# Kernel optimization log

Hardware: AMD Instinct MI355X
Metric: run time of the kernel (lower is better)

The kernel has to match this reference:

```python
import jax, jax.numpy as jnp
import numpy as np

DT = 10.0          # ms per step
T_STEPS = 120      # rollout length
THRESHOLD = 0.5
MIX = 0.0          # competition_mix (buffer, default 0.0)
EPS_TOTAL = 1e-6
EPS_SLOPE = 1e-3
NOISE_SEED = 42


def setup_inputs() -> dict:
    key = jax.random.key(0)
    B, C = 65536, 4
    logits = jax.random.normal(key, (B, C), dtype=jnp.float32)
    return {
        "logits": logits,
        "input_scale": jnp.float32(0.25),
        "leak": jnp.full((C,), 0.08, dtype=jnp.float32),
        "self_excitation": jnp.full((C,), 0.12, dtype=jnp.float32),
        "inhibition": jnp.float32(0.08),
        "competition_gain": jnp.float32(1.0),
        "noise_std": jnp.float32(0.02),
        "evidence_w": jnp.float32(1.0),   # evidence_proj: Linear(1,1) weight
        "evidence_b": jnp.float32(0.0),   # evidence_proj bias
    }


def _forward(logits, input_scale, leak, self_excitation, inhibition,
             competition_gain, noise_std, evidence_w, evidence_b):
    B, C = logits.shape
    # momentary evidence: scale, center, softplus, 1x1 linear
    centered = logits * input_scale
    centered = centered - jnp.mean(centered, axis=1, keepdims=True)
    evidence = jax.nn.softplus(centered) * evidence_w + evidence_b  # (B, C)

    lk = jax.nn.softplus(leak)                # (C,)
    se = jax.nn.softplus(self_excitation)     # (C,)
    inhib = jax.nn.softplus(inhibition)       # ()
    cgain = jax.nn.softplus(competition_gain) # ()
    nstd = jax.nn.softplus(noise_std)         # ()

    keys = jax.random.split(jax.random.key(NOISE_SEED), T_STEPS)

    def step(acc, k):
        total = jnp.sum(acc, axis=1, keepdims=True)      # (B, 1)
        total_other = total - acc                        # (B, C)
        normalized_other = total_other / (total + EPS_TOTAL)
        competition = (1.0 - MIX) * total_other + MIX * cgain * normalized_other
        drive = evidence + se * acc - inhib * competition - lk * acc
        noise = jax.random.normal(k, (B, C), dtype=jnp.float32) * nstd
        dsdt = jax.nn.softplus(drive + noise) - acc
        acc_new = jnp.maximum(acc + 0.2 * dsdt, 0.0)     # clamp(min=0)
        return acc_new, (acc_new, dsdt)

    acc0 = jnp.zeros((B, C), dtype=jnp.float32)
    _, (traj, dsdt_traj) = jax.lax.scan(step, acc0, keys)
    traj = jnp.transpose(traj, (1, 0, 2))           # (B, T, C)
    dsdt_traj = jnp.transpose(dsdt_traj, (1, 0, 2)) # (B, T, C)

    # DiffDecisionMultiClass: first threshold crossing per class, with
    # linear interpolation using dsdt (slope = 0.2*dsdt per step) so the
    # decision time is differentiable via the implicit-function gradient.
    diff = traj - THRESHOLD                          # (B, T, C)
    crossed = diff > 0.0
    any_c = jnp.any(crossed, axis=1)                 # (B, C)
    idx = jnp.argmax(crossed, axis=1)                # (B, C) first crossing step
    idx = jnp.where(any_c, idx, T_STEPS - 1)

    diff_c = jnp.take_along_axis(diff, idx[:, None, :], axis=1)[:, 0, :]       # (B, C)
    slope = 0.2 * jnp.take_along_axis(dsdt_traj, idx[:, None, :], axis=1)[:, 0, :]
    slope_safe = jnp.where(slope >= 0.0,
                           jnp.maximum(slope, EPS_SLOPE),
                           jnp.minimum(slope, -EPS_SLOPE))
    # continuous crossing time in steps (gradient flows through diff_c only)
    t_cont = idx.astype(jnp.float32) - diff_c / jax.lax.stop_gradient(slope_safe)
    times_ms = jnp.where(any_c, t_cont * DT, jnp.float32(T_STEPS * DT))
    return times_ms / 1000.0  # seconds, (B, C)


def reference(logits, input_scale, leak, self_excitation, inhibition,
              competition_gain, noise_std, evidence_w, evidence_b):
    return _forward(logits, input_scale, leak, self_excitation, inhibition,
                    competition_gain, noise_std, evidence_w, evidence_b)
```

## Files before the change

### kernel.cpp

```cpp
#include <hip/hip_runtime.h>
#include <cstdint>

#define TSTEPS 120
#define KPAD   (TSTEPS + 4)

typedef unsigned int u32;

constexpr u32 rotl_c(u32 x, u32 r) { return (x << r) | (x >> (32u - r)); }

struct KeyTab { u32 w[KPAD][2]; };

constexpr KeyTab make_tab() {
    KeyTab kt{};
    for (int t = 0; t < KPAD; ++t) {
        const u32 k0 = 0u, k1 = 42u, ks2 = k0 ^ k1 ^ 0x1BD11BDAu;
        u32 x0 = k0, x1 = (u32)t + k1;
        const u32 rA[4] = {13u, 15u, 26u, 6u};
        const u32 rB[4] = {17u, 29u, 16u, 24u};
        for (int g = 0; g < 5; ++g) {
            const u32* rr = (g % 2 == 0) ? rA : rB;
            for (int i = 0; i < 4; ++i) { x0 += x1; x1 = rotl_c(x1, rr[i]); x1 ^= x0; }
            switch (g) {
                case 0: x0 += k1;  x1 += ks2 + 1u; break;
                case 1: x0 += ks2; x1 += k0 + 2u;  break;
                case 2: x0 += k0;  x1 += k1 + 3u;  break;
                case 3: x0 += k1;  x1 += ks2 + 4u; break;
                case 4: x0 += ks2; x1 += k0 + 5u;  break;
            }
        }
        kt.w[t][0] = x0; kt.w[t][1] = x1;
    }
    return kt;
}

__constant__ KeyTab KT = make_tab();

__device__ __forceinline__ u32 rotl32(u32 x, u32 r) { return (x << r) | (x >> (32u - r)); }

__device__ __forceinline__ float qxor1(float x) {
    return __int_as_float(__builtin_amdgcn_update_dpp(0, __float_as_int(x), 0xB1, 0xF, 0xF, true));
}
__device__ __forceinline__ float qxor2(float x) {
    return __int_as_float(__builtin_amdgcn_update_dpp(0, __float_as_int(x), 0x4E, 0xF, 0xF, true));
}

__device__ __forceinline__ float softplus_s(float x) {
    const float LOG2E = 1.4426950408889634f, LN2 = 0.6931471805599453f;
    float e = __builtin_amdgcn_exp2f(-fabsf(x) * LOG2E);
    return fmaxf(x, 0.0f) + __builtin_amdgcn_logf(1.0f + e) * LN2;
}

__device__ __forceinline__ float erfinv_fast(float x) {
    const float LN2 = 0.6931471805599453f;
    float t = __builtin_fmaf(-x, x, 1.0f);
    float w = __builtin_amdgcn_logf(t) * (-LN2);
    float wa = w - 2.5f;
    float p = 2.81022636e-08f;
    p = fmaf(p, wa, 3.43273939e-07f);
    p = fmaf(p, wa, -3.5233877e-06f);
    p = fmaf(p, wa, -4.39150654e-06f);
    p = fmaf(p, wa, 0.00021858087f);
    p = fmaf(p, wa, -0.00125372503f);
    p = fmaf(p, wa, -0.00417768164f);
    p = fmaf(p, wa, 0.246640727f);
    p = fmaf(p, wa, 1.50140941f);
    if (__any(w >= 5.0f)) {
        float wb = __builtin_amdgcn_sqrtf(w) - 3.0f;
        float q = -0.000200214257f;
        q = fmaf(q, wb, 0.000100950558f);
        q = fmaf(q, wb, 0.00134934322f);
        q = fmaf(q, wb, -0.00367342844f);
        q = fmaf(q, wb, 0.00573950773f);
        q = fmaf(q, wb, -0.0076224613f);
        q = fmaf(q, wb, 0.00943887047f);
        q = fmaf(q, wb, 1.00167406f);
        q = fmaf(q, wb, 2.83297682f);
        p = (w < 5.0f) ? p : q;
    }
    return p * x;
}

__device__ __forceinline__ u32 tf_bits(int t, u32 c) {
    const u32 k0 = KT.w[t][0], k1 = KT.w[t][1];
    const u32 ks2 = k0 ^ k1 ^ 0x1BD11BDAu;
    const u32 i1 = ks2 + 1u, i2 = k0 + 2u, i3 = k1 + 3u, i4 = ks2 + 4u, i5 = k0 + 5u;
    u32 x0 = k0, x1 = c + k1;
#define TF_R(r) { x0 += x1; x1 = rotl32(x1, (r)); x1 ^= x0; }
    TF_R(13u) TF_R(15u) TF_R(26u) TF_R(6u)
    x0 += k1;  x1 += i1;
    TF_R(17u) TF_R(29u) TF_R(16u) TF_R(24u)
    x0 += ks2; x1 += i2;
    TF_R(13u) TF_R(15u) TF_R(26u) TF_R(6u)
    x0 += k0;  x1 += i3;
    TF_R(17u) TF_R(29u) TF_R(16u) TF_R(24u)
    x0 += k1;  x1 += i4;
    TF_R(13u) TF_R(15u) TF_R(26u) TF_R(6u)
    x0 += ks2; x1 += i5;
#undef TF_R
    return x0 ^ x1;
}

__global__ __launch_bounds__(256, 4) void accrace_kernel(
    const float* __restrict__ logits,
    const float* __restrict__ g_input_scale,
    const float* __restrict__ g_leak,
    const float* __restrict__ g_se,
    const float* __restrict__ g_inhib,
    const float* __restrict__ g_nstd,
    const float* __restrict__ g_ew,
    const float* __restrict__ g_eb,
    float* __restrict__ out, int n)
{
    const int tid = threadIdx.x;
    const int j = blockIdx.x * 256 + tid;
    if (j >= n) return;
    const int c = tid & 3;

    const float input_scale = g_input_scale[0];
    const float lkc   = softplus_s(g_leak[c]);
    const float sec   = softplus_s(g_se[c]);
    const float inhib = softplus_s(g_inhib[0]);
    const float nstd  = softplus_s(g_nstd[0]);
    const float ew = g_ew[0], eb = g_eb[0];

    const float gain   = sec + inhib - lkc;
    const float minhib = -inhib;
    const float SQ2N   = 1.41421356237309515f * nstd;
    const float LO     = -0.99999994f;

    const float xs = logits[j] * input_scale;
    float m = xs + qxor1(xs); m = (m + qxor2(m)) * 0.25f;
    const float evd = softplus_s(xs - m) * ew + eb;

    const u32 ctr = (u32)j;

    float nz;
    u32 bitsa;
    {
        const u32 b0 = tf_bits(0, ctr);
        const float F0 = __uint_as_float((b0 >> 9) | 0x3F800000u);
        const float u0 = fmaxf(fmaf(F0, 2.0f, -3.0f), LO);
        nz = erfinv_fast(u0) * SQ2N;
        bitsa = tf_bits(1, ctr);
    }

    float acc = 0.0f, dfx = 0.0f, slx = 0.0f;
    int idxv = -1;

#pragma unroll 4
    for (int t = 0; t < TSTEPS; ++t) {
        float s1  = acc + qxor1(acc);
        float tot = s1 + qxor2(s1);
        const float dr = fmaf(acc, gain, fmaf(tot, minhib, evd));
        const float sp = softplus_s(dr + nz);
        const float ds = sp - acc;
        const float an = fmaxf(fmaf(ds, 0.2f, acc), 0.0f);

        const bool cr = (idxv < 0) & (an > 0.5f);
        idxv = cr ? t : idxv;
        dfx  = cr ? an : dfx;
        slx  = cr ? ds : slx;
        acc = an;

        const float F = __uint_as_float((bitsa >> 9) | 0x3F800000u);
        const float u = fmaxf(fmaf(F, 2.0f, -3.0f), LO);
        nz = erfinv_fast(u) * SQ2N;
        bitsa = tf_bits(t + 2, ctr);
    }

    float o = 1.2f;
    if (idxv >= 0) {
        const float sl = 0.2f * slx;
        const float ss = (sl >= 0.0f) ? fmaxf(sl, 1e-3f) : fminf(sl, -1e-3f);
        o = (((float)idxv - (dfx - 0.5f) / ss) * 10.0f) / 1000.0f;
    }
    out[j] = o;
}

extern "C" void kernel_launch(void* const* d_in, const int* in_sizes, int n_in,
                              void* d_out, int out_size, void* d_ws, size_t ws_size,
                              hipStream_t stream) {
    const float* logits       = (const float*)d_in[0];
    const float* input_scale  = (const float*)d_in[1];
    const float* leak         = (const float*)d_in[2];
    const float* self_excit   = (const float*)d_in[3];
    const float* inhibition   = (const float*)d_in[4];
    const float* noise_std    = (const float*)d_in[6];
    const float* evidence_w   = (const float*)d_in[7];
    const float* evidence_b   = (const float*)d_in[8];

    const int n = in_sizes[0];
    const int threads = 256;
    const int blocks = (n + threads - 1) / threads;
    accrace_kernel<<<blocks, threads, 0, stream>>>(
        logits, input_scale, leak, self_excit, inhibition,
        noise_std, evidence_w, evidence_b, (float*)d_out, n);
}
```

Measured before the change: 88.73 us.

## Batch noise generation per 15-step tile and make erfinv branchless

```diff
diff --git a/kernel.cpp b/kernel.cpp
--- a/kernel.cpp
+++ b/kernel.cpp
@@ -2,17 +2,18 @@
 #include <cstdint>
 
 #define TSTEPS 120
-#define KPAD   (TSTEPS + 4)
+#define TTILE  15
+#define NTILES (TSTEPS / TTILE)
 
 typedef unsigned int u32;
 
 constexpr u32 rotl_c(u32 x, u32 r) { return (x << r) | (x >> (32u - r)); }
 
-struct KeyTab { u32 w[KPAD][2]; };
+struct KeyTab { u32 w[TSTEPS][2]; };
 
 constexpr KeyTab make_tab() {
     KeyTab kt{};
-    for (int t = 0; t < KPAD; ++t) {
+    for (int t = 0; t < TSTEPS; ++t) {
         const u32 k0 = 0u, k1 = 42u, ks2 = k0 ^ k1 ^ 0x1BD11BDAu;
         u32 x0 = k0, x1 = (u32)t + k1;
         const u32 rA[4] = {13u, 15u, 26u, 6u};
@@ -37,6 +38,10 @@
 
 __device__ __forceinline__ u32 rotl32(u32 x, u32 r) { return (x << r) | (x >> (32u - r)); }
 
+__device__ __forceinline__ float rfl(float x) {
+    return __int_as_float(__builtin_amdgcn_readfirstlane(__float_as_int(x)));
+}
+
 __device__ __forceinline__ float qxor1(float x) {
     return __int_as_float(__builtin_amdgcn_update_dpp(0, __float_as_int(x), 0xB1, 0xF, 0xF, true));
 }
@@ -50,33 +55,22 @@
     return fmaxf(x, 0.0f) + __builtin_amdgcn_logf(1.0f + e) * LN2;
 }
 
-__device__ __forceinline__ float erfinv_fast(float x) {
+__device__ __forceinline__ float erfinv_bl(float x) {
     const float LN2 = 0.6931471805599453f;
     float t = __builtin_fmaf(-x, x, 1.0f);
     float w = __builtin_amdgcn_logf(t) * (-LN2);
     float wa = w - 2.5f;
-    float p = 2.81022636e-08f;
-    p = fmaf(p, wa, 3.43273939e-07f);
-    p = fmaf(p, wa, -3.5233877e-06f);
-    p = fmaf(p, wa, -4.39150654e-06f);
-    p = fmaf(p, wa, 0.00021858087f);
-    p = fmaf(p, wa, -0.00125372503f);
-    p = fmaf(p, wa, -0.00417768164f);
-    p = fmaf(p, wa, 0.246640727f);
-    p = fmaf(p, wa, 1.50140941f);
-    if (__any(w >= 5.0f)) {
-        float wb = __builtin_amdgcn_sqrtf(w) - 3.0f;
-        float q = -0.000200214257f;
-        q = fmaf(q, wb, 0.000100950558f);
-        q = fmaf(q, wb, 0.00134934322f);
-        q = fmaf(q, wb, -0.00367342844f);
-        q = fmaf(q, wb, 0.00573950773f);
-        q = fmaf(q, wb, -0.0076224613f);
-        q = fmaf(q, wb, 0.00943887047f);
-        q = fmaf(q, wb, 1.00167406f);
-        q = fmaf(q, wb, 2.83297682f);
-        p = (w < 5.0f) ? p : q;
-    }
+    float wb = __builtin_amdgcn_sqrtf(w) - 3.0f;
+    float p = 2.81022636e-08f;           float q = -0.000200214257f;
+    p = fmaf(p, wa, 3.43273939e-07f);    q = fmaf(q, wb, 0.000100950558f);
+    p = fmaf(p, wa, -3.5233877e-06f);    q = fmaf(q, wb, 0.00134934322f);
+    p = fmaf(p, wa, -4.39150654e-06f);   q = fmaf(q, wb, -0.00367342844f);
+    p = fmaf(p, wa, 0.00021858087f);     q = fmaf(q, wb, 0.00573950773f);
+    p = fmaf(p, wa, -0.00125372503f);    q = fmaf(q, wb, -0.0076224613f);
+    p = fmaf(p, wa, -0.00417768164f);    q = fmaf(q, wb, 0.00943887047f);
+    p = fmaf(p, wa, 0.246640727f);       q = fmaf(q, wb, 1.00167406f);
+    p = fmaf(p, wa, 1.50140941f);        q = fmaf(q, wb, 2.83297682f);
+    p = (w < 5.0f) ? p : q;
     return p * x;
 }
 
@@ -119,13 +113,13 @@
     const float input_scale = g_input_scale[0];
     const float lkc   = softplus_s(g_leak[c]);
     const float sec   = softplus_s(g_se[c]);
-    const float inhib = softplus_s(g_inhib[0]);
-    const float nstd  = softplus_s(g_nstd[0]);
+    const float inhib = rfl(softplus_s(g_inhib[0]));
+    const float nstd  = rfl(softplus_s(g_nstd[0]));
     const float ew = g_ew[0], eb = g_eb[0];
 
     const float gain   = sec + inhib - lkc;
     const float minhib = -inhib;
-    const float SQ2N   = 1.41421356237309515f * nstd;
+    const float SQ2N   = rfl(1.41421356237309515f * nstd);
     const float LO     = -0.99999994f;
 
     const float xs = logits[j] * input_scale;
@@ -134,38 +128,36 @@
 
     const u32 ctr = (u32)j;
 
-    float nz;
-    u32 bitsa;
-    {
-        const u32 b0 = tf_bits(0, ctr);
-        const float F0 = __uint_as_float((b0 >> 9) | 0x3F800000u);
-        const float u0 = fmaxf(fmaf(F0, 2.0f, -3.0f), LO);
-        nz = erfinv_fast(u0) * SQ2N;
-        bitsa = tf_bits(1, ctr);
-    }
-
     float acc = 0.0f, dfx = 0.0f, slx = 0.0f;
     int idxv = -1;
+    float nzv[TTILE];
 
-#pragma unroll 4
-    for (int t = 0; t < TSTEPS; ++t) {
-        float s1  = acc + qxor1(acc);
-        float tot = s1 + qxor2(s1);
-        const float dr = fmaf(acc, gain, fmaf(tot, minhib, evd));
-        const float sp = softplus_s(dr + nz);
-        const float ds = sp - acc;
-        const float an = fmaxf(fmaf(ds, 0.2f, acc), 0.0f);
+    for (int tile = 0; tile < NTILES; ++tile) {
+        const int t0 = tile * TTILE;
 
-        const bool cr = (idxv < 0) & (an > 0.5f);
-        idxv = cr ? t : idxv;
-        dfx  = cr ? an : dfx;
-        slx  = cr ? ds : slx;
-        acc = an;
+#pragma unroll
+        for (int tt = 0; tt < TTILE; ++tt) {
+            const u32 bits = tf_bits(t0 + tt, ctr);
+            const float F = __uint_as_float((bits >> 9) | 0x3F800000u);
+            const float u = fmaxf(fmaf(F, 2.0f, -3.0f), LO);
+            nzv[tt] = erfinv_bl(u) * SQ2N;
+        }
 
-        const float F = __uint_as_float((bitsa >> 9) | 0x3F800000u);
-        const float u = fmaxf(fmaf(F, 2.0f, -3.0f), LO);
-        nz = erfinv_fast(u) * SQ2N;
-        bitsa = tf_bits(t + 2, ctr);
+#pragma unroll
+        for (int tt = 0; tt < TTILE; ++tt) {
+            float s1  = acc + qxor1(acc);
+            float tot = s1 + qxor2(s1);
+            const float dr = fmaf(acc, gain, fmaf(tot, minhib, evd));
+            const float sp = softplus_s(dr + nzv[tt]);
+            const float ds = sp - acc;
+            const float an = fmaxf(fmaf(ds, 0.2f, acc), 0.0f);
+
+            const bool cr = (idxv < 0) & (an > 0.5f);
+            idxv = cr ? (t0 + tt) : idxv;
+            dfx  = cr ? an : dfx;
+            slx  = cr ? ds : slx;
+            acc = an;
+        }
     }
 
     float o = 1.2f;
```

Result: slower. 90.68 us (+2.2%).
